# Kernel optimization log

Hardware: AMD Instinct MI355X
Metric: run time of the kernel (lower is better)

Reference implementation:

```python
import jax, jax.numpy as jnp
import numpy as np

V, E, H, M, NE, K, HH = 32000, 512, 1024, 64, 8, 2, 512
B, S = 2, 2048


def gif(u, decay=0.9, thresh=1.0):
    """GIF spiking neuron: leaky-integrate membrane with soft (surrogate) spike.
    u: [B, S, H] input current. Returns spikes [B, S, H]."""
    def step(v, ut):
        v = decay * v + ut
        s = jax.nn.sigmoid(4.0 * (v - thresh))  # surrogate spike
        return v - s * thresh, s                  # soft reset
    v0 = jnp.zeros(u.shape[:1] + u.shape[2:], u.dtype)
    _, sp = jax.lax.scan(step, v0, jnp.swapaxes(u, 0, 1))
    return jnp.swapaxes(sp, 0, 1)


def setup_inputs() -> dict:
    key = jax.random.key(0)
    ks = jax.random.split(key, 12)
    r = lambda k, shp, s: jax.random.normal(k, shp, dtype=jnp.float32) * s
    z = lambda shp: jnp.zeros(shp, jnp.float32)
    return {
        "input_ids": jax.random.randint(ks[0], (B, S), 0, V),
        "emb": r(ks[1], (V, E), 0.02),
        "enc_W": r(ks[2], (E, H), 0.05), "enc_b": z((H,)),
        "s2c_W": r(ks[3], (H, M), 0.05), "s2c_b": z((M,)),
        "rW1": r(ks[4], (M, 64), 0.1), "rb1": z((64,)),
        "rW2": r(ks[5], (64, NE), 0.1), "rb2": z((NE,)),
        "eW1": r(ks[6], (NE, M, HH), 0.05), "eb1": z((NE, HH)),
        "eW2": r(ks[7], (NE, HH), 0.05), "eb2": z((NE,)),
        "c2s_W": r(ks[8], (M, H), 0.05), "c2s_b": z((H,)),
        "dec_W": r(ks[9], (H, E), 0.05), "dec_b": z((E,)),
        "out_W": r(ks[10], (E, V), 0.02), "out_b": z((V,)),
    }


def reference(input_ids, emb, enc_W, enc_b, s2c_W, s2c_b, rW1, rb1, rW2, rb2,
              eW1, eb1, eW2, eb2, c2s_W, c2s_b, dec_W, dec_b, out_W, out_b):
    x = emb[input_ids]                                  # [B,S,E] embedding gather
    sp_enc = gif(x @ enc_W + enc_b)                     # [B,S,H] GIF encoder
    cont = sp_enc @ s2c_W + s2c_b                       # [B,S,M] spike->continuous (rate)
    # Liquid MoE router: gating MLP -> softmax -> top-k
    gl = jnp.tanh(cont @ rW1 + rb1) @ rW2 + rb2
    gates = jax.nn.softmax(gl, axis=-1)                 # [B,S,NE]
    topg, topi = jax.lax.top_k(gates, K)
    topg = topg / jnp.sum(topg, axis=-1, keepdims=True)
    # SNN experts: scalar prediction per token per expert (dense, scalar output)
    h = jnp.tanh(jnp.einsum('bsm,emh->bseh', cont, eW1) + eb1)  # [B,S,NE,HH]
    eo = jnp.einsum('bseh,eh->bse', h, eW2) + eb2               # [B,S,NE]
    y = jnp.sum(topg * jnp.take_along_axis(eo, topi, axis=-1), axis=-1)  # [B,S]
    # scalar y_hat repeated to moe_hidden_dim, as in forward_async
    y_rep = jnp.broadcast_to(y[..., None], y.shape + (M,))      # [B,S,M]
    # continuous->spike (poisson): deterministic expected rate, mean over spike steps
    rate = jax.nn.sigmoid(y_rep @ c2s_W + c2s_b)                # [B,S,H]
    dec = gif(rate @ dec_W + dec_b)                             # [B,S,E] GIF decoder
    return dec @ out_W + out_b                                  # [B,S,V]
```

## Files before the change

### kernel.cpp

```cpp
#include <hip/hip_runtime.h>
#include <hip/hip_bf16.h>
#include <stdint.h>

typedef __attribute__((ext_vector_type(8))) short bf16x8;
typedef __attribute__((ext_vector_type(4))) float f32x4;
typedef __attribute__((address_space(3))) char lds_char_t;

#define LOG2E_X2 2.885390081777927f
#define GIF_A 5.770780163555854f

__device__ __forceinline__ float fexp2(float x) { return __builtin_amdgcn_exp2f(x); }
__device__ __forceinline__ float frcp(float x)  { return __builtin_amdgcn_rcpf(x); }
__device__ __forceinline__ float gif_spike(float v) {
  return frcp(1.f + fexp2(fmaf(v, -GIF_A, GIF_A)));
}
__device__ __forceinline__ float fsig(float x)  { return frcp(1.f + fexp2(-1.442695040888963f * x)); }
__device__ __forceinline__ float ftanh(float x) { return 1.f - 2.f * frcp(1.f + fexp2(LOG2E_X2 * x)); }
__device__ __forceinline__ float b2f(unsigned short u) {
  return __uint_as_float((unsigned)u << 16);
}

__device__ __forceinline__ void gload_lds16(const void* g, void* l) {
  __builtin_amdgcn_global_load_lds((__attribute__((address_space(1))) void*)(uintptr_t)g,
                                   (__attribute__((address_space(3))) void*)l, 16, 0, 0);
}

__device__ __forceinline__ bf16x8 ds_read_b128_asm(unsigned addr) {
  bf16x8 r;
  asm volatile("ds_read_b128 %0, %1" : "=v"(r) : "v"(addr));
  return r;
}

__device__ __forceinline__ void transpose_body(const float* __restrict__ in,
                                               __hip_bfloat16* __restrict__ out,
                                               int K, int N, int bx, int by,
                                               float (*tile)[33], int tid) {
  int n0 = bx * 32, k0 = by * 32;
  int tx = tid & 31, ty = tid >> 5;
#pragma unroll
  for (int i = 0; i < 4; ++i)
    tile[ty + 8 * i][tx] = in[(size_t)(k0 + ty + 8 * i) * N + n0 + tx];
  __syncthreads();
#pragma unroll
  for (int i = 0; i < 4; ++i)
    out[(size_t)(n0 + ty + 8 * i) * K + k0 + tx] = __float2bfloat16(tile[tx][ty + 8 * i]);
}

__global__ __launch_bounds__(256) void prep_k(
    const float* __restrict__ enc_W, __hip_bfloat16* __restrict__ encWt,
    const float* __restrict__ dec_W, __hip_bfloat16* __restrict__ decWt,
    const float* __restrict__ eW1, __hip_bfloat16* __restrict__ eW1b,
    const int* __restrict__ ids, const float* __restrict__ emb,
    __hip_bfloat16* __restrict__ Aenc,
    const float* __restrict__ c2s_W, float* __restrict__ csum) {
  __shared__ float tile[32][33];
  int bid = blockIdx.x;
  int tid = threadIdx.x;
  if (bid < 512) {
    transpose_body(enc_W, encWt, 512, 1024, bid % 32, bid / 32, tile, tid);
  } else if (bid < 1024) {
    int b = bid - 512;
    transpose_body(dec_W, decWt, 1024, 512, b % 16, b / 16, tile, tid);
  } else if (bid < 1280) {
    int i = (bid - 1024) * 256 + tid;
    float4 v = ((const float4*)eW1)[i];
    __hip_bfloat16* o = eW1b + i * 4;
    o[0] = __float2bfloat16(v.x); o[1] = __float2bfloat16(v.y);
    o[2] = __float2bfloat16(v.z); o[3] = __float2bfloat16(v.w);
  } else if (bid < 3328) {
    int i = (bid - 1280) * 256 + tid;
    int idx = i * 4;
    int row = idx >> 9, col = idx & 511;
    float4 v = *(const float4*)(emb + (size_t)ids[row] * 512 + col);
    __hip_bfloat16* o = Aenc + idx;
    o[0] = __float2bfloat16(v.x); o[1] = __float2bfloat16(v.y);
    o[2] = __float2bfloat16(v.z); o[3] = __float2bfloat16(v.w);
  } else {
    int h = (bid - 3328) * 256 + tid;
    float a = 0.f;
#pragma unroll 8
    for (int m = 0; m < 64; ++m) a += c2s_W[m * 1024 + h];
    csum[h] = a;
  }
}

__global__ __launch_bounds__(256) void gif_trans_k(
    const float* __restrict__ u, float* __restrict__ sp,
    const float* __restrict__ out_W, __hip_bfloat16* __restrict__ outWt) {
  __shared__ float tile[32][33];
  int bid = blockIdx.x;
  int tid = threadIdx.x;
  if (bid >= 128) {
    int b = bid - 128;
    transpose_body(out_W, outWt, 512, 32000, b % 1000, b / 1000, tile, tid);
    return;
  }
  const int S = 2048, C = 1024;
  int chunk = bid >> 3;
  int gc = (bid & 7) * 256 + tid;
  int b = (gc >= C) ? 1 : 0, ch = gc - b * C;
  size_t base = (size_t)b * S * C + ch;

  const int CH = 128;
  int s_begin = chunk * CH;
  int sw = (chunk == 0) ? 0 : s_begin - 96;
  int warm = s_begin - sw;
  int total = CH + warm;
  const float* up = u + base + (size_t)sw * C;

  float v = 0.f;
  float bufA[16], bufB[16];
#pragma unroll
  for (int i = 0; i < 16; ++i) bufA[i] = up[(size_t)i * C];
  for (int t = 0; t < total; t += 32) {
#pragma unroll
    for (int i = 0; i < 16; ++i) bufB[i] = up[(size_t)(t + 16 + i) * C];
#pragma unroll
    for (int i = 0; i < 16; ++i) {
      v = fmaf(0.9f, v, bufA[i]);
      float spk = gif_spike(v);
      v -= spk;
      if (t + i >= warm) sp[base + (size_t)(sw + t + i) * C] = spk;
    }
    if (t + 32 < total) {
#pragma unroll
      for (int i = 0; i < 16; ++i) bufA[i] = up[(size_t)(t + 32 + i) * C];
    }
#pragma unroll
    for (int i = 0; i < 16; ++i) {
      v = fmaf(0.9f, v, bufB[i]);
      float spk = gif_spike(v);
      v -= spk;
      if (t + 16 + i >= warm) sp[base + (size_t)(sw + t + 16 + i) * C] = spk;
    }
  }
}

__global__ __launch_bounds__(256) void gemm128_k(
    const __hip_bfloat16* __restrict__ A, const __hip_bfloat16* __restrict__ Bt,
    const float* __restrict__ bias, float* __restrict__ C, int N, int K, int GM) {
  __shared__ __align__(16) char smem[65536];

  int nwg = gridDim.x;
  int bid = blockIdx.x;
  int q = nwg >> 3, r = nwg & 7, xcd = bid & 7, bix = bid >> 3;
  int wg = (xcd < r ? xcd * (q + 1) : r * (q + 1) + (xcd - r) * q) + bix;
  int bm = wg % GM, bn = wg / GM;

  int tid = threadIdx.x;
  int lane = tid & 63, w = tid >> 6;
  int wm = w >> 1, wn = w & 1;

  const __hip_bfloat16* gA[4];
  const __hip_bfloat16* gB[4];
#pragma unroll
  for (int i = 0; i < 4; ++i) {
    int c = (w * 4 + i) * 64 + lane;
    int rr = c >> 3, sl = c & 7;
    int sg = sl ^ (rr & 7);
    gA[i] = A + (size_t)(bm * 128 + rr) * K + sg * 8;
    gB[i] = Bt + (size_t)(bn * 128 + rr) * K + sg * 8;
  }

  f32x4 acc[4][4];
#pragma unroll
  for (int i = 0; i < 4; ++i)
#pragma unroll
    for (int j = 0; j < 4; ++j) acc[i][j] = (f32x4){0.f, 0.f, 0.f, 0.f};

  auto stage = [&](int kt, int b) {
    int ko = kt * 64;
    char* baseA = smem + b * 32768;
    char* baseB = baseA + 16384;
#pragma unroll
    for (int i = 0; i < 4; ++i) {
      gload_lds16(gA[i] + ko, baseA + (w * 4 + i) * 1024);
      gload_lds16(gB[i] + ko, baseB + (w * 4 + i) * 1024);
    }
  };

  const int KT = K >> 6;
  stage(0, 0);
  asm volatile("s_waitcnt vmcnt(0)" ::: "memory");
  __builtin_amdgcn_s_barrier();
  int cur = 0;
  for (int kt = 0; kt < KT; ++kt) {
    if (kt + 1 < KT) {
      stage(kt + 1, cur ^ 1);
      asm volatile("s_waitcnt vmcnt(8)" ::: "memory");
    } else {
      asm volatile("s_waitcnt vmcnt(0)" ::: "memory");
    }
    __builtin_amdgcn_s_barrier();
    const char* smA = smem + cur * 32768;
    const char* smB = smA + 16384;
#pragma unroll
    for (int ks = 0; ks < 2; ++ks) {
      bf16x8 af[4], bfr[4];
#pragma unroll
      for (int f = 0; f < 4; ++f) {
        int R = wm * 64 + f * 16 + (lane & 15);
        int R2 = wn * 64 + f * 16 + (lane & 15);
        int sg = ks * 4 + (lane >> 4);
        af[f]  = *(const bf16x8*)(smA + R * 128 + ((sg ^ (R & 7)) << 4));
        bfr[f] = *(const bf16x8*)(smB + R2 * 128 + ((sg ^ (R2 & 7)) << 4));
      }
#pragma unroll
      for (int fm = 0; fm < 4; ++fm)
#pragma unroll
        for (int fn = 0; fn < 4; ++fn)
          acc[fm][fn] = __builtin_amdgcn_mfma_f32_16x16x32_bf16(af[fm], bfr[fn], acc[fm][fn], 0, 0, 0);
    }
    __builtin_amdgcn_sched_barrier(0);
    __builtin_amdgcn_s_barrier();
    cur ^= 1;
  }
  int rbase = bm * 128 + wm * 64 + ((lane >> 4) << 2);
  int cbase = bn * 128 + wn * 64 + (lane & 15);
#pragma unroll
  for (int fn = 0; fn < 4; ++fn) {
    int col = cbase + fn * 16;
    float bs = bias[col];
#pragma unroll
    for (int fm = 0; fm < 4; ++fm) {
      int row = rbase + fm * 16;
#pragma unroll
      for (int rr = 0; rr < 4; ++rr)
        C[(size_t)(row + rr) * N + col] = acc[fm][fn][rr] + bs;
    }
  }
}

__global__ __launch_bounds__(512, 2) void gemm256_k(
    const __hip_bfloat16* __restrict__ A, const __hip_bfloat16* __restrict__ Bt,
    const float* __restrict__ bias, float* __restrict__ C, int N, int K) {
  __shared__ __align__(16) char smem[131072];

  int nwg = gridDim.x;
  int bid = blockIdx.x;
  int q = nwg >> 3, r = nwg & 7, xcd = bid & 7, bix = bid >> 3;
  int wg = (xcd < r ? xcd * (q + 1) : r * (q + 1) + (xcd - r) * q) + bix;
  int S  = wg / 1000;
  int rr_ = wg - S * 1000;
  int g  = rr_ / 40;
  int t  = rr_ - g * 40;
  int bn = g * 5 + (t >> 3);
  int bm = S * 8 + (t & 7);

  int tid = threadIdx.x;
  int lane = tid & 63, w = tid >> 6;
  int wm = w >> 2, wn = w & 3;

  int offA[4], offB[4];
#pragma unroll
  for (int i = 0; i < 4; ++i) {
    int c = (w * 4 + i) * 64 + lane;
    int rw = c >> 3, sl = c & 7;
    int sg = sl ^ (rw & 7);
    offA[i] = (bm * 256 + rw) * K + sg * 8;
    offB[i] = rw * K + sg * 8;
  }
  const __hip_bfloat16* Bb = Bt + (size_t)(bn * 256) * K;

  f32x4 acc[8][4];
#pragma unroll
  for (int i = 0; i < 8; ++i)
#pragma unroll
    for (int j = 0; j < 4; ++j) acc[i][j] = (f32x4){0.f, 0.f, 0.f, 0.f};

  auto stage = [&](int kt, int b) {
    int ko = kt * 64;
    char* baseA = smem + b * 65536;
    char* baseB = baseA + 32768;
#pragma unroll
    for (int i = 0; i < 4; ++i) {
      gload_lds16(A + offA[i] + ko, baseA + (w * 4 + i) * 1024);
      gload_lds16(Bb + offB[i] + ko, baseB + (w * 4 + i) * 1024);
    }
  };

  unsigned sbase = (unsigned)(uintptr_t)(lds_char_t*)smem;

  const int KT = K >> 6;
  stage(0, 0);
  int cur = 0;
  for (int kt = 0; kt < KT; ++kt) {
    if (kt + 1 < KT) {
      stage(kt + 1, cur ^ 1);
      asm volatile("s_waitcnt vmcnt(8)" ::: "memory");
    } else {
      asm volatile("s_waitcnt vmcnt(0)" ::: "memory");
    }
    __builtin_amdgcn_s_barrier();
    unsigned aA = sbase + cur * 65536;
    unsigned aB = aA + 32768;
    int sg0 = (lane >> 4);
    int sg1 = 4 + (lane >> 4);

    bf16x8 b0[4], b1[4], a0a[4], a0b[4], a1a[4], a1b[4];
#pragma unroll
    for (int f = 0; f < 4; ++f) {
      int R2 = wn * 64 + f * 16 + (lane & 15);
      b0[f] = ds_read_b128_asm(aB + R2 * 128 + ((sg0 ^ (R2 & 7)) << 4));
    }
#pragma unroll
    for (int f = 0; f < 4; ++f) {
      int R = wm * 128 + f * 16 + (lane & 15);
      a0a[f] = ds_read_b128_asm(aA + R * 128 + ((sg0 ^ (R & 7)) << 4));
    }
#pragma unroll
    for (int f = 0; f < 4; ++f) {
      int R = wm * 128 + (f + 4) * 16 + (lane & 15);
      a0b[f] = ds_read_b128_asm(aA + R * 128 + ((sg0 ^ (R & 7)) << 4));
    }
#pragma unroll
    for (int f = 0; f < 4; ++f) {
      int R2 = wn * 64 + f * 16 + (lane & 15);
      b1[f] = ds_read_b128_asm(aB + R2 * 128 + ((sg1 ^ (R2 & 7)) << 4));
    }
#pragma unroll
    for (int f = 0; f < 4; ++f) {
      int R = wm * 128 + f * 16 + (lane & 15);
      a1a[f] = ds_read_b128_asm(aA + R * 128 + ((sg1 ^ (R & 7)) << 4));
    }
#pragma unroll
    for (int f = 0; f < 4; ++f) {
      int R = wm * 128 + (f + 4) * 16 + (lane & 15);
      a1b[f] = ds_read_b128_asm(aA + R * 128 + ((sg1 ^ (R & 7)) << 4));
    }
    asm volatile("s_waitcnt lgkmcnt(12)" ::: "memory");
    __builtin_amdgcn_sched_barrier(0);
    __builtin_amdgcn_s_setprio(1);
#pragma unroll
    for (int fm = 0; fm < 4; ++fm)
#pragma unroll
      for (int fn = 0; fn < 4; ++fn)
        acc[fm][fn] = __builtin_amdgcn_mfma_f32_16x16x32_bf16(a0a[fm], b0[fn], acc[fm][fn], 0, 0, 0);
#pragma unroll
    for (int fm = 0; fm < 4; ++fm)
#pragma unroll
      for (int fn = 0; fn < 4; ++fn)
        acc[fm + 4][fn] = __builtin_amdgcn_mfma_f32_16x16x32_bf16(a0b[fm], b0[fn], acc[fm + 4][fn], 0, 0, 0);
    __builtin_amdgcn_s_setprio(0);
    asm volatile("s_waitcnt lgkmcnt(0)" ::: "memory");
    __builtin_amdgcn_sched_barrier(0);
    __builtin_amdgcn_s_setprio(1);
#pragma unroll
    for (int fm = 0; fm < 4; ++fm)
#pragma unroll
      for (int fn = 0; fn < 4; ++fn)
        acc[fm][fn] = __builtin_amdgcn_mfma_f32_16x16x32_bf16(a1a[fm], b1[fn], acc[fm][fn], 0, 0, 0);
#pragma unroll
    for (int fm = 0; fm < 4; ++fm)
#pragma unroll
      for (int fn = 0; fn < 4; ++fn)
        acc[fm + 4][fn] = __builtin_amdgcn_mfma_f32_16x16x32_bf16(a1b[fm], b1[fn], acc[fm + 4][fn], 0, 0, 0);
    __builtin_amdgcn_s_setprio(0);
    __builtin_amdgcn_sched_barrier(0);
    __builtin_amdgcn_s_barrier();
    cur ^= 1;
  }

  float* sC = (float*)smem;
#pragma unroll
  for (int h = 0; h < 2; ++h) {
    __syncthreads();
    if (wm == h) {
#pragma unroll
      for (int fn = 0; fn < 4; ++fn) {
        int lc = wn * 64 + fn * 16 + (lane & 15);
        float bs = bias[bn * 256 + lc];
#pragma unroll
        for (int fm = 0; fm < 8; ++fm)
#pragma unroll
          for (int rw = 0; rw < 4; ++rw) {
            int lr = fm * 16 + ((lane >> 4) << 2) + rw;
            sC[lr * 256 + lc] = acc[fm][fn][rw] + bs;
          }
      }
    }
    __syncthreads();
#pragma unroll
    for (int it = 0; it < 16; ++it) {
      int lr = it * 8 + w;
      int lc = (tid & 63) * 4;
      float4 v = *(float4*)&sC[lr * 256 + lc];
      *(float4*)(C + (size_t)(bm * 256 + h * 128 + lr) * N + bn * 256 + lc) = v;
    }
  }
}

__global__ void gif_scan_k(const float* __restrict__ u, __hip_bfloat16* __restrict__ out,
                           int S, int C, int bpc) {
  int chunk = blockIdx.x / bpc;
  int gc = (blockIdx.x - chunk * bpc) * 64 + threadIdx.x;
  int b = (gc >= C) ? 1 : 0, ch = gc - b * C;
  size_t base = (size_t)b * S * C + ch;

  const int CH = 128;
  int s_begin = chunk * CH;
  int sw = (chunk == 0) ? 0 : s_begin - 96;
  int warm = s_begin - sw;
  int total = CH + warm;
  const float* up = u + base + (size_t)sw * C;

  float v = 0.f;
  float bufA[16], bufB[16];
#pragma unroll
  for (int i = 0; i < 16; ++i) bufA[i] = up[(size_t)i * C];
  for (int t = 0; t < total; t += 32) {
#pragma unroll
    for (int i = 0; i < 16; ++i) bufB[i] = up[(size_t)(t + 16 + i) * C];
#pragma unroll
    for (int i = 0; i < 16; ++i) {
      v = fmaf(0.9f, v, bufA[i]);
      float spk = gif_spike(v);
      v -= spk;
      if (t + i >= warm) out[base + (size_t)(sw + t + i) * C] = __float2bfloat16(spk);
    }
    if (t + 32 < total) {
#pragma unroll
      for (int i = 0; i < 16; ++i) bufA[i] = up[(size_t)(t + 32 + i) * C];
    }
#pragma unroll
    for (int i = 0; i < 16; ++i) {
      v = fmaf(0.9f, v, bufB[i]);
      float spk = gif_spike(v);
      v -= spk;
      if (t + 16 + i >= warm) out[base + (size_t)(sw + t + 16 + i) * C] = __float2bfloat16(spk);
    }
  }
}

__global__ void s2c_k(const float* __restrict__ sp, const float* __restrict__ W,
                      const float* __restrict__ b, float* __restrict__ cont) {
  int n = threadIdx.x & 63, tg = threadIdx.x >> 6;
  int tok0 = blockIdx.x * 16 + tg * 4;
  const float* s0 = sp + (size_t)tok0 * 1024;
  float a0 = 0, a1 = 0, a2 = 0, a3 = 0;
#pragma unroll 8
  for (int k = 0; k < 1024; ++k) {
    float w = W[k * 64 + n];
    a0 += s0[k] * w;
    a1 += s0[k + 1024] * w;
    a2 += s0[k + 2048] * w;
    a3 += s0[k + 3072] * w;
  }
  float bb = b[n];
  cont[(size_t)(tok0 + 0) * 64 + n] = a0 + bb;
  cont[(size_t)(tok0 + 1) * 64 + n] = a1 + bb;
  cont[(size_t)(tok0 + 2) * 64 + n] = a2 + bb;
  cont[(size_t)(tok0 + 3) * 64 + n] = a3 + bb;
}

__global__ __launch_bounds__(512) void moe_k(
    const float* __restrict__ cont,
    const float* __restrict__ rW1, const float* __restrict__ rb1,
    const float* __restrict__ rW2, const float* __restrict__ rb2,
    const __hip_bfloat16* __restrict__ eW1b, const float* __restrict__ eb1,
    const float* __restrict__ eW2, const float* __restrict__ eb2,
    const float* __restrict__ csum, const float* __restrict__ c2sb,
    __hip_bfloat16* __restrict__ rate) {
  __shared__ float sc[16][65];
  __shared__ float sh1[16][65];
  __shared__ float sgl[16][8];
  __shared__ float seo[16][8];
  __shared__ float sy[16];
  int tid = threadIdx.x;
  int t0 = blockIdx.x * 16;

  for (int i = tid; i < 1024; i += 512) sc[i >> 6][i & 63] = cont[(size_t)t0 * 64 + i];
  __syncthreads();

  if (tid < 256) {
    int tok = tid >> 4, u0 = tid & 15;
#pragma unroll
    for (int uu = 0; uu < 4; ++uu) {
      int un = u0 + 16 * uu;
      float a = rb1[un];
#pragma unroll 8
      for (int m = 0; m < 64; ++m) a += sc[tok][m] * rW1[m * 64 + un];
      sh1[tok][un] = ftanh(a);
    }
  }
  __syncthreads();
  if (tid < 128) {
    int tok = tid >> 3, e = tid & 7;
    float a = rb2[e];
#pragma unroll 8
    for (int j = 0; j < 64; ++j) a += sh1[tok][j] * rW2[j * 8 + e];
    sgl[tok][e] = a;
  }
  __syncthreads();

  {
    int jj = tid & 63, e = tid >> 6;
    float eop[16];
#pragma unroll
    for (int t = 0; t < 16; ++t) eop[t] = 0.f;
#pragma unroll
    for (int jr = 0; jr < 2; ++jr) {
      int j = jj * 4 + jr * 256;
      float4 bb = *(const float4*)(eb1 + e * 512 + j);
      float4 a[16];
#pragma unroll
      for (int t = 0; t < 16; ++t) a[t] = bb;
      const ushort4* wp = (const ushort4*)(eW1b + (size_t)e * 64 * 512 + j);
#pragma unroll 4
      for (int m = 0; m < 64; ++m) {
        ushort4 wu = wp[(size_t)m * 128];
        float wx = b2f(wu.x), wy = b2f(wu.y), wz = b2f(wu.z), ww = b2f(wu.w);
#pragma unroll
        for (int t = 0; t < 16; ++t) {
          float c = sc[t][m];
          a[t].x += wx * c; a[t].y += wy * c;
          a[t].z += wz * c; a[t].w += ww * c;
        }
      }
      float4 w2 = *(const float4*)(eW2 + e * 512 + j);
#pragma unroll
      for (int t = 0; t < 16; ++t)
        eop[t] += ftanh(a[t].x) * w2.x + ftanh(a[t].y) * w2.y +
                  ftanh(a[t].z) * w2.z + ftanh(a[t].w) * w2.w;
    }
#pragma unroll
    for (int t = 0; t < 16; ++t) {
#pragma unroll
      for (int off = 32; off > 0; off >>= 1) eop[t] += __shfl_down(eop[t], off);
    }
    if (jj == 0) {
      float b2 = eb2[e];
#pragma unroll
      for (int t = 0; t < 16; ++t) seo[t][e] = eop[t] + b2;
    }
  }
  __syncthreads();

  if (tid < 16) {
    int tok = tid;
    float mx = sgl[tok][0];
#pragma unroll
    for (int e = 1; e < 8; ++e) mx = fmaxf(mx, sgl[tok][e]);
#pragma unroll
    for (int e = 0; e < 8; ++e) sgl[tok][e] = __expf(sgl[tok][e] - mx);
    int i0 = 0;
#pragma unroll
    for (int e = 1; e < 8; ++e) if (sgl[tok][e] > sgl[tok][i0]) i0 = e;
    int i1 = (i0 == 0) ? 1 : 0;
#pragma unroll
    for (int e = 0; e < 8; ++e) if (e != i0 && sgl[tok][e] > sgl[tok][i1]) i1 = e;
    float g0 = sgl[tok][i0], g1 = sgl[tok][i1];
    sy[tok] = (g0 * seo[tok][i0] + g1 * seo[tok][i1]) / (g0 + g1);
  }
  __syncthreads();

  for (int i = tid; i < 16 * 1024; i += 512) {
    int tok = i >> 10, h = i & 1023;
    float r = fsig(sy[tok] * csum[h] + c2sb[h]);
    rate[(size_t)(t0 + tok) * 1024 + h] = __float2bfloat16(r);
  }
}

extern "C" void kernel_launch(void* const* d_in, const int* in_sizes, int n_in,
                              void* d_out, int out_size, void* d_ws, size_t ws_size,
                              hipStream_t stream) {
  (void)in_sizes; (void)n_in; (void)out_size; (void)ws_size;
  const int*   ids   = (const int*)d_in[0];
  const float* emb   = (const float*)d_in[1];
  const float* enc_W = (const float*)d_in[2];
  const float* enc_b = (const float*)d_in[3];
  const float* s2c_W = (const float*)d_in[4];
  const float* s2c_b = (const float*)d_in[5];
  const float* rW1   = (const float*)d_in[6];
  const float* rb1   = (const float*)d_in[7];
  const float* rW2   = (const float*)d_in[8];
  const float* rb2   = (const float*)d_in[9];
  const float* eW1   = (const float*)d_in[10];
  const float* eb1   = (const float*)d_in[11];
  const float* eW2   = (const float*)d_in[12];
  const float* eb2   = (const float*)d_in[13];
  const float* c2s_W = (const float*)d_in[14];
  const float* c2s_b = (const float*)d_in[15];
  const float* dec_W = (const float*)d_in[16];
  const float* dec_b = (const float*)d_in[17];
  const float* out_W = (const float*)d_in[18];
  const float* out_b = (const float*)d_in[19];
  float* out = (float*)d_out;

  char* ws = (char*)d_ws;
  size_t off = 0;
  auto alloc = [&](size_t bytes) -> char* {
    off = (off + 255) & ~(size_t)255;
    char* p = ws + off;
    off += bytes;
    return p;
  };
  __hip_bfloat16* outWt = (__hip_bfloat16*)alloc(32000ull * 512 * 2);
  __hip_bfloat16* encWt = (__hip_bfloat16*)alloc(1024ull * 512 * 2);
  __hip_bfloat16* decWt = (__hip_bfloat16*)alloc(512ull * 1024 * 2);
  __hip_bfloat16* eW1b  = (__hip_bfloat16*)alloc(8ull * 64 * 512 * 2);
  __hip_bfloat16* Aenc  = (__hip_bfloat16*)alloc(4096ull * 512 * 2);
  float* u_enc  = (float*)alloc(4096ull * 1024 * 4);
  float* sp_enc = (float*)alloc(4096ull * 1024 * 4);
  float* cont   = (float*)alloc(4096ull * 64 * 4);
  float* csum   = (float*)alloc(1024 * 4);
  float* u_dec  = (float*)alloc(4096ull * 512 * 4);
  __hip_bfloat16* dec = (__hip_bfloat16*)alloc(4096ull * 512 * 2);
  __hip_bfloat16* rate = (__hip_bfloat16*)u_enc;

  prep_k<<<3332, 256, 0, stream>>>(enc_W, encWt, dec_W, decWt,
                                   eW1, eW1b, ids, emb, Aenc, c2s_W, csum);

  gemm128_k<<<32 * 8, 256, 0, stream>>>(Aenc, encWt, enc_b, u_enc, 1024, 512, 32);
  gif_trans_k<<<128 + 16000, 256, 0, stream>>>(u_enc, sp_enc, out_W, outWt);
  s2c_k<<<256, 256, 0, stream>>>(sp_enc, s2c_W, s2c_b, cont);
  moe_k<<<256, 512, 0, stream>>>(cont, rW1, rb1, rW2, rb2, eW1b, eb1, eW2, eb2, csum, c2s_b, rate);
  gemm128_k<<<32 * 4, 256, 0, stream>>>(rate, decWt, dec_b, u_dec, 512, 1024, 32);
  gif_scan_k<<<16 * 16, 64, 0, stream>>>(u_dec, dec, 2048, 512, 16);
  gemm256_k<<<2000, 512, 0, stream>>>(dec, outWt, out_b, out, 32000, 512);
}
```

Baseline: 432.4 us.

## Use 4-wave 128x128 warp tiles in output GEMM and 64x64 weight transpose

The output-projection GEMM drops from 8 waves to 4 waves per 256x256 block. Each wave now computes a 128x128 sub-tile with 8x8 MFMA fragments per k-step, which raises register reuse and halves the LDS reads per MFMA. The out_W transpose-and-cast moves to 64x64 tiles with float4 loads and short4 stores, so it launches fewer blocks and moves wider vectors. The trade-offs are a large accumulator (256 VGPRs of accumulators) at occupancy 1, fewer waves to hide latency, and the loss of the split lgkmcnt overlap that the old k-loop had.

After: 454.1 us. +5.0%, slower.

```diff
diff --git a/kernel.cpp b/kernel.cpp
--- a/kernel.cpp
+++ b/kernel.cpp
@@ -87,12 +87,31 @@
 __global__ __launch_bounds__(256) void gif_trans_k(
     const float* __restrict__ u, float* __restrict__ sp,
     const float* __restrict__ out_W, __hip_bfloat16* __restrict__ outWt) {
-  __shared__ float tile[32][33];
+  __shared__ float tile[64][65];
   int bid = blockIdx.x;
   int tid = threadIdx.x;
   if (bid >= 128) {
     int b = bid - 128;
-    transpose_body(out_W, outWt, 512, 32000, b % 1000, b / 1000, tile, tid);
+    int n0 = (b % 500) * 64, k0 = (b / 500) * 64;
+    int kg = tid >> 4, nf = tid & 15;
+#pragma unroll
+    for (int i = 0; i < 4; ++i) {
+      int kr = kg + 16 * i;
+      float4 v = *(const float4*)(out_W + (size_t)(k0 + kr) * 32000 + n0 + nf * 4);
+      tile[nf * 4 + 0][kr] = v.x;
+      tile[nf * 4 + 1][kr] = v.y;
+      tile[nf * 4 + 2][kr] = v.z;
+      tile[nf * 4 + 3][kr] = v.w;
+    }
+    __syncthreads();
+#pragma unroll
+    for (int i = 0; i < 4; ++i) {
+      int nr = kg + 16 * i;
+      float4 v = *(const float4*)&tile[nr][nf * 4];
+      __hip_bfloat16 o[4] = {__float2bfloat16(v.x), __float2bfloat16(v.y),
+                             __float2bfloat16(v.z), __float2bfloat16(v.w)};
+      *(short4*)(outWt + (size_t)(n0 + nr) * 512 + k0 + nf * 4) = *(short4*)o;
+    }
     return;
   }
   const int S = 2048, C = 1024;
@@ -231,7 +250,7 @@
   }
 }
 
-__global__ __launch_bounds__(512, 2) void gemm256_k(
+__global__ __launch_bounds__(256, 1) void gemm256_k(
     const __hip_bfloat16* __restrict__ A, const __hip_bfloat16* __restrict__ Bt,
     const float* __restrict__ bias, float* __restrict__ C, int N, int K) {
   __shared__ __align__(16) char smem[131072];
@@ -249,12 +268,12 @@
 
   int tid = threadIdx.x;
   int lane = tid & 63, w = tid >> 6;
-  int wm = w >> 2, wn = w & 3;
-
-  int offA[4], offB[4];
-#pragma unroll
-  for (int i = 0; i < 4; ++i) {
-    int c = (w * 4 + i) * 64 + lane;
+  int wm = w >> 1, wn = w & 1;
+
+  int offA[8], offB[8];
+#pragma unroll
+  for (int i = 0; i < 8; ++i) {
+    int c = (w * 8 + i) * 64 + lane;
     int rw = c >> 3, sl = c & 7;
     int sg = sl ^ (rw & 7);
     offA[i] = (bm * 256 + rw) * K + sg * 8;
@@ -262,20 +281,20 @@
   }
   const __hip_bfloat16* Bb = Bt + (size_t)(bn * 256) * K;
 
-  f32x4 acc[8][4];
+  f32x4 acc[8][8];
 #pragma unroll
   for (int i = 0; i < 8; ++i)
 #pragma unroll
-    for (int j = 0; j < 4; ++j) acc[i][j] = (f32x4){0.f, 0.f, 0.f, 0.f};
+    for (int j = 0; j < 8; ++j) acc[i][j] = (f32x4){0.f, 0.f, 0.f, 0.f};
 
   auto stage = [&](int kt, int b) {
     int ko = kt * 64;
     char* baseA = smem + b * 65536;
     char* baseB = baseA + 32768;
 #pragma unroll
-    for (int i = 0; i < 4; ++i) {
-      gload_lds16(A + offA[i] + ko, baseA + (w * 4 + i) * 1024);
-      gload_lds16(Bb + offB[i] + ko, baseB + (w * 4 + i) * 1024);
+    for (int i = 0; i < 8; ++i) {
+      gload_lds16(A + offA[i] + ko, baseA + (w * 8 + i) * 1024);
+      gload_lds16(Bb + offB[i] + ko, baseB + (w * 8 + i) * 1024);
     }
   };
 
@@ -287,75 +306,37 @@
   for (int kt = 0; kt < KT; ++kt) {
     if (kt + 1 < KT) {
       stage(kt + 1, cur ^ 1);
-      asm volatile("s_waitcnt vmcnt(8)" ::: "memory");
+      asm volatile("s_waitcnt vmcnt(16)" ::: "memory");
     } else {
       asm volatile("s_waitcnt vmcnt(0)" ::: "memory");
     }
     __builtin_amdgcn_s_barrier();
     unsigned aA = sbase + cur * 65536;
     unsigned aB = aA + 32768;
-    int sg0 = (lane >> 4);
-    int sg1 = 4 + (lane >> 4);
-
-    bf16x8 b0[4], b1[4], a0a[4], a0b[4], a1a[4], a1b[4];
-#pragma unroll
-    for (int f = 0; f < 4; ++f) {
-      int R2 = wn * 64 + f * 16 + (lane & 15);
-      b0[f] = ds_read_b128_asm(aB + R2 * 128 + ((sg0 ^ (R2 & 7)) << 4));
-    }
-#pragma unroll
-    for (int f = 0; f < 4; ++f) {
-      int R = wm * 128 + f * 16 + (lane & 15);
-      a0a[f] = ds_read_b128_asm(aA + R * 128 + ((sg0 ^ (R & 7)) << 4));
-    }
-#pragma unroll
-    for (int f = 0; f < 4; ++f) {
-      int R = wm * 128 + (f + 4) * 16 + (lane & 15);
-      a0b[f] = ds_read_b128_asm(aA + R * 128 + ((sg0 ^ (R & 7)) << 4));
-    }
-#pragma unroll
-    for (int f = 0; f < 4; ++f) {
-      int R2 = wn * 64 + f * 16 + (lane & 15);
-      b1[f] = ds_read_b128_asm(aB + R2 * 128 + ((sg1 ^ (R2 & 7)) << 4));
-    }
-#pragma unroll
-    for (int f = 0; f < 4; ++f) {
-      int R = wm * 128 + f * 16 + (lane & 15);
-      a1a[f] = ds_read_b128_asm(aA + R * 128 + ((sg1 ^ (R & 7)) << 4));
-    }
-#pragma unroll
-    for (int f = 0; f < 4; ++f) {
-      int R = wm * 128 + (f + 4) * 16 + (lane & 15);
-      a1b[f] = ds_read_b128_asm(aA + R * 128 + ((sg1 ^ (R & 7)) << 4));
-    }
-    asm volatile("s_waitcnt lgkmcnt(12)" ::: "memory");
-    __builtin_amdgcn_sched_barrier(0);
-    __builtin_amdgcn_s_setprio(1);
-#pragma unroll
-    for (int fm = 0; fm < 4; ++fm)
-#pragma unroll
-      for (int fn = 0; fn < 4; ++fn)
-        acc[fm][fn] = __builtin_amdgcn_mfma_f32_16x16x32_bf16(a0a[fm], b0[fn], acc[fm][fn], 0, 0, 0);
-#pragma unroll
-    for (int fm = 0; fm < 4; ++fm)
-#pragma unroll
-      for (int fn = 0; fn < 4; ++fn)
-        acc[fm + 4][fn] = __builtin_amdgcn_mfma_f32_16x16x32_bf16(a0b[fm], b0[fn], acc[fm + 4][fn], 0, 0, 0);
-    __builtin_amdgcn_s_setprio(0);
-    asm volatile("s_waitcnt lgkmcnt(0)" ::: "memory");
-    __builtin_amdgcn_sched_barrier(0);
-    __builtin_amdgcn_s_setprio(1);
-#pragma unroll
-    for (int fm = 0; fm < 4; ++fm)
-#pragma unroll
-      for (int fn = 0; fn < 4; ++fn)
-        acc[fm][fn] = __builtin_amdgcn_mfma_f32_16x16x32_bf16(a1a[fm], b1[fn], acc[fm][fn], 0, 0, 0);
-#pragma unroll
-    for (int fm = 0; fm < 4; ++fm)
-#pragma unroll
-      for (int fn = 0; fn < 4; ++fn)
-        acc[fm + 4][fn] = __builtin_amdgcn_mfma_f32_16x16x32_bf16(a1b[fm], b1[fn], acc[fm + 4][fn], 0, 0, 0);
-    __builtin_amdgcn_s_setprio(0);
+#pragma unroll
+    for (int ks = 0; ks < 2; ++ks) {
+      int sg = ks * 4 + (lane >> 4);
+      bf16x8 af[8], bfr[8];
+#pragma unroll
+      for (int f = 0; f < 8; ++f) {
+        int R = wm * 128 + f * 16 + (lane & 15);
+        af[f] = ds_read_b128_asm(aA + R * 128 + ((sg ^ (R & 7)) << 4));
+      }
+#pragma unroll
+      for (int f = 0; f < 8; ++f) {
+        int R2 = wn * 128 + f * 16 + (lane & 15);
+        bfr[f] = ds_read_b128_asm(aB + R2 * 128 + ((sg ^ (R2 & 7)) << 4));
+      }
+      asm volatile("s_waitcnt lgkmcnt(0)" ::: "memory");
+      __builtin_amdgcn_sched_barrier(0);
+      __builtin_amdgcn_s_setprio(1);
+#pragma unroll
+      for (int fm = 0; fm < 8; ++fm)
+#pragma unroll
+        for (int fn = 0; fn < 8; ++fn)
+          acc[fm][fn] = __builtin_amdgcn_mfma_f32_16x16x32_bf16(af[fm], bfr[fn], acc[fm][fn], 0, 0, 0);
+      __builtin_amdgcn_s_setprio(0);
+    }
     __builtin_amdgcn_sched_barrier(0);
     __builtin_amdgcn_s_barrier();
     cur ^= 1;
@@ -367,8 +348,8 @@
     __syncthreads();
     if (wm == h) {
 #pragma unroll
-      for (int fn = 0; fn < 4; ++fn) {
-        int lc = wn * 64 + fn * 16 + (lane & 15);
+      for (int fn = 0; fn < 8; ++fn) {
+        int lc = wn * 128 + fn * 16 + (lane & 15);
         float bs = bias[bn * 256 + lc];
 #pragma unroll
         for (int fm = 0; fm < 8; ++fm)
@@ -381,8 +362,8 @@
     }
     __syncthreads();
 #pragma unroll
-    for (int it = 0; it < 16; ++it) {
-      int lr = it * 8 + w;
+    for (int it = 0; it < 32; ++it) {
+      int lr = it * 4 + (tid >> 6);
       int lc = (tid & 63) * 4;
       float4 v = *(float4*)&sC[lr * 256 + lc];
       *(float4*)(C + (size_t)(bm * 256 + h * 128 + lr) * N + bn * 256 + lc) = v;
@@ -612,10 +593,10 @@
                                    eW1, eW1b, ids, emb, Aenc, c2s_W, csum);
 
   gemm128_k<<<32 * 8, 256, 0, stream>>>(Aenc, encWt, enc_b, u_enc, 1024, 512, 32);
-  gif_trans_k<<<128 + 16000, 256, 0, stream>>>(u_enc, sp_enc, out_W, outWt);
+  gif_trans_k<<<128 + 4000, 256, 0, stream>>>(u_enc, sp_enc, out_W, outWt);
   s2c_k<<<256, 256, 0, stream>>>(sp_enc, s2c_W, s2c_b, cont);
   moe_k<<<256, 512, 0, stream>>>(cont, rW1, rb1, rW2, rb2, eW1b, eb1, eW2, eb2, csum, c2s_b, rate);
   gemm128_k<<<32 * 4, 256, 0, stream>>>(rate, decWt, dec_b, u_dec, 512, 1024, 32);
   gif_scan_k<<<16 * 16, 64, 0, stream>>>(u_dec, dec, 2048, 512, 16);
-  gemm256_k<<<2000, 512, 0, stream>>>(dec, outWt, out_b, out, 32000, 512);
-}
+  gemm256_k<<<2000, 256, 0, stream>>>(dec, outWt, out_b, out, 32000, 512);
+}
```
